# Kernel optimization log

Hardware: AMD Instinct MI355X
Metric: run time of the kernel (lower is better)

Reference implementation:

```python
import jax, jax.numpy as jnp
import numpy as np

IN_DIM, HID, OUT_DIM = 128, 24, 4096
B, K = 16384, 256

def setup_inputs() -> dict:
    key = jax.random.key(0)
    ks = jax.random.split(key, 8)
    x = jax.random.normal(ks[0], (B, IN_DIM), dtype=jnp.float32)
    possible_moves = jax.random.randint(ks[1], (B, K), 0, OUT_DIM)
    s1 = 1.0 / np.sqrt(IN_DIM)
    s2 = 1.0 / np.sqrt(HID)
    W1 = jax.random.uniform(ks[2], (IN_DIM, HID), jnp.float32, -s1, s1)
    b1 = jax.random.uniform(ks[3], (HID,), jnp.float32, -s1, s1)
    W2 = jax.random.uniform(ks[4], (HID, HID), jnp.float32, -s2, s2)
    b2 = jax.random.uniform(ks[5], (HID,), jnp.float32, -s2, s2)
    W3 = jax.random.uniform(ks[6], (HID, OUT_DIM), jnp.float32, -s2, s2)
    b3 = jax.random.uniform(ks[7], (OUT_DIM,), jnp.float32, -s2, s2)
    return {"x": x, "possible_moves": possible_moves,
            "W1": W1, "b1": b1, "W2": W2, "b2": b2, "W3": W3, "b3": b3}

def reference(x, possible_moves, W1, b1, W2, b2, W3, b3):
    # small MLP: 128 -> 24 -> 24 -> 4096
    h = jax.nn.relu(x @ W1 + b1)
    h = jax.nn.relu(h @ W2 + b2)
    logits = h @ W3 + b3                     # [B, OUT_DIM]
    # per-row legal-move mask via vectorized scatter (duplicates just re-set 1)
    Bn = logits.shape[0]
    rows = jnp.arange(Bn)[:, None]           # [B, 1] broadcasts over K
    mask = jnp.zeros_like(logits).at[rows, possible_moves].set(1.0)
    # faithful to original: multiply (not -inf) then softmax over full dim
    filtered = logits * mask
    return jax.nn.softmax(filtered, axis=1)
```

## Files before the change

kernel.cpp:

```cpp
#include <hip/hip_runtime.h>
#include <hip/hip_bf16.h>

#define IN_DIM 128
#define HID 24
#define OUT_DIM 4096
#define NB 16384
#define KMOV 256

#define TR_BLOCKS 384
#define MLP_BLOCKS (NB / 8)

__global__ __launch_bounds__(256) void kprep(const float* __restrict__ x,
                                             const float* __restrict__ W1,
                                             const float* __restrict__ b1,
                                             const float* __restrict__ W2,
                                             const float* __restrict__ b2,
                                             const float* __restrict__ W3,
                                             float* __restrict__ W3T,
                                             float* __restrict__ h2out) {
    __shared__ float W1s[IN_DIM * HID];
    __shared__ float W2s[HID * HID];
    __shared__ float b1s[HID], b2s[HID];
    __shared__ float xs[8][IN_DIM];

    int bid = blockIdx.x;
    int t = threadIdx.x;

    if (bid < TR_BLOCKS) {
        int i = bid * 256 + t;
        int c = i / HID;
        int k = i - c * HID;
        W3T[i] = W3[k * OUT_DIM + c];
        return;
    }

    for (int i = t; i < IN_DIM * HID; i += 256) W1s[i] = W1[i];
    for (int i = t; i < HID * HID; i += 256)    W2s[i] = W2[i];
    if (t < HID) { b1s[t] = b1[t]; b2s[t] = b2[t]; }
    int rbase = (bid - TR_BLOCKS) * 8;
    for (int i = t; i < 8 * IN_DIM; i += 256)
        xs[i >> 7][i & 127] = x[(size_t)rbase * IN_DIM + i];
    __syncthreads();

    int g = t >> 5;
    int j = t & 31;
    int r = rbase + g;

    float h1 = 0.f;
    if (j < HID) {
        h1 = b1s[j];
        #pragma unroll 8
        for (int i = 0; i < IN_DIM; i++) h1 += xs[g][i] * W1s[i * HID + j];
        h1 = fmaxf(h1, 0.f);
    }
    float h2 = (j < HID) ? b2s[j] : 0.f;
    #pragma unroll
    for (int k = 0; k < HID; k++) {
        float hk = __shfl(h1, k, 32);
        if (j < HID) h2 += hk * W2s[k * HID + j];
    }
    if (j < HID) {
        h2 = fmaxf(h2, 0.f);
        h2out[(size_t)r * HID + j] = h2;
    }
}

__global__ __launch_bounds__(256) void kmain2(const int* __restrict__ moves,
                                              const float* __restrict__ b3,
                                              const float* __restrict__ W3T,
                                              const float* __restrict__ h2all,
                                              float* __restrict__ out) {
    __shared__ __align__(16) float probs[OUT_DIM];
    __shared__ float h2s[HID];
    __shared__ float red[8];
    unsigned char* claimed = (unsigned char*)probs;

    int r = blockIdx.x;
    int t = threadIdx.x;

    int c = moves[(size_t)r * KMOV + t];
    if (t < HID) h2s[t] = h2all[(size_t)r * HID + t];
    __syncthreads();

    const float4* w = (const float4*)(W3T + c * HID);
    float4 a0 = w[0], a1 = w[1], a2 = w[2], a3 = w[3], a4 = w[4], a5 = w[5];
    float acc = b3[c];
    acc += a0.x*h2s[0] + a0.y*h2s[1] + a0.z*h2s[2]  + a0.w*h2s[3];
    acc += a1.x*h2s[4] + a1.y*h2s[5] + a1.z*h2s[6]  + a1.w*h2s[7];
    acc += a2.x*h2s[8] + a2.y*h2s[9] + a2.z*h2s[10] + a2.w*h2s[11];
    acc += a3.x*h2s[12]+ a3.y*h2s[13]+ a3.z*h2s[14] + a3.w*h2s[15];
    acc += a4.x*h2s[16]+ a4.y*h2s[17]+ a4.z*h2s[18] + a4.w*h2s[19];
    acc += a5.x*h2s[20]+ a5.y*h2s[21]+ a5.z*h2s[22] + a5.w*h2s[23];

    claimed[c] = (unsigned char)t;

    float m = acc;
    #pragma unroll
    for (int off = 32; off > 0; off >>= 1) m = fmaxf(m, __shfl_xor(m, off, 64));
    int wid = t >> 6;
    if ((t & 63) == 0) red[wid] = m;
    __syncthreads();
    float mm = fmaxf(fmaxf(fmaxf(red[0], red[1]), fmaxf(red[2], red[3])), 0.f);

    float e      = __expf(acc - mm);
    float base_e = __expf(-mm);

    float contrib = (claimed[c] == (unsigned char)t) ? (e - base_e) : 0.f;
    float s = contrib;
    #pragma unroll
    for (int off = 32; off > 0; off >>= 1) s += __shfl_xor(s, off, 64);
    if ((t & 63) == 0) red[4 + wid] = s;
    __syncthreads();
    float denom = (float)OUT_DIM * base_e + (red[4] + red[5] + red[6] + red[7]);
    float inv = 1.0f / denom;
    float oc  = base_e * inv;
    float pm  = e * inv;

    float4* p4 = (float4*)probs;
    float4 ocv = make_float4(oc, oc, oc, oc);
    #pragma unroll
    for (int i = 0; i < 4; i++) p4[t + i * 256] = ocv;
    __syncthreads();
    probs[c] = pm;
    __syncthreads();

    float4* out4 = (float4*)(out + (size_t)r * OUT_DIM);
    #pragma unroll
    for (int i = 0; i < 4; i++) out4[t + i * 256] = p4[t + i * 256];
}

extern "C" void kernel_launch(void* const* d_in, const int* in_sizes, int n_in,
                              void* d_out, int out_size, void* d_ws, size_t ws_size,
                              hipStream_t stream) {
    const float* x     = (const float*)d_in[0];
    const int*   moves = (const int*)  d_in[1];
    const float* W1    = (const float*)d_in[2];
    const float* b1    = (const float*)d_in[3];
    const float* W2    = (const float*)d_in[4];
    const float* b2    = (const float*)d_in[5];
    const float* W3    = (const float*)d_in[6];
    const float* b3    = (const float*)d_in[7];
    float* out = (float*)d_out;

    char* ws = (char*)d_ws;
    float* W3T = (float*)ws;
    float* h2  = (float*)(ws + OUT_DIM * HID * 4);

    kprep<<<TR_BLOCKS + MLP_BLOCKS, 256, 0, stream>>>(x, W1, b1, W2, b2, W3, W3T, h2);
    kmain2<<<NB, 256, 0, stream>>>(moves, b3, W3T, h2, out);
}
```

Measured before the change: 329.9 us.

## Dedupe moves via zeroed LDS scatter and store outputs nontemporally

Replaces the byte-claim dedup trick with zero-initialising the shared probability row, scattering exp(acc-max)-base per move, then having each thread read its float4 slice back to form the sum and the final output. This removes one barrier and the separate fill-then-scatter pass before the copy-out. Output writes now use nontemporal vector stores to avoid cache pollution for the large streaming output. It also moves the b3 load before the first barrier to overlap latency.

```diff
diff --git a/kernel.cpp b/kernel.cpp
--- a/kernel.cpp
+++ b/kernel.cpp
@@ -9,6 +9,8 @@
 
 #define TR_BLOCKS 384
 #define MLP_BLOCKS (NB / 8)
+
+typedef float f32x4 __attribute__((ext_vector_type(4)));
 
 __global__ __launch_bounds__(256) void kprep(const float* __restrict__ x,
                                              const float* __restrict__ W1,
@@ -73,26 +75,30 @@
     __shared__ __align__(16) float probs[OUT_DIM];
     __shared__ float h2s[HID];
     __shared__ float red[8];
-    unsigned char* claimed = (unsigned char*)probs;
 
     int r = blockIdx.x;
     int t = threadIdx.x;
 
     int c = moves[(size_t)r * KMOV + t];
     if (t < HID) h2s[t] = h2all[(size_t)r * HID + t];
-    __syncthreads();
 
     const float4* w = (const float4*)(W3T + c * HID);
     float4 a0 = w[0], a1 = w[1], a2 = w[2], a3 = w[3], a4 = w[4], a5 = w[5];
-    float acc = b3[c];
+    float bc = b3[c];
+    __syncthreads();
+
+    float4* p4 = (float4*)probs;
+    float4 z = make_float4(0.f, 0.f, 0.f, 0.f);
+    #pragma unroll
+    for (int i = 0; i < 4; i++) p4[t + i * 256] = z;
+
+    float acc = bc;
     acc += a0.x*h2s[0] + a0.y*h2s[1] + a0.z*h2s[2]  + a0.w*h2s[3];
     acc += a1.x*h2s[4] + a1.y*h2s[5] + a1.z*h2s[6]  + a1.w*h2s[7];
     acc += a2.x*h2s[8] + a2.y*h2s[9] + a2.z*h2s[10] + a2.w*h2s[11];
     acc += a3.x*h2s[12]+ a3.y*h2s[13]+ a3.z*h2s[14] + a3.w*h2s[15];
     acc += a4.x*h2s[16]+ a4.y*h2s[17]+ a4.z*h2s[18] + a4.w*h2s[19];
     acc += a5.x*h2s[20]+ a5.y*h2s[21]+ a5.z*h2s[22] + a5.w*h2s[23];
-
-    claimed[c] = (unsigned char)t;
 
     float m = acc;
     #pragma unroll
@@ -102,31 +108,33 @@
     __syncthreads();
     float mm = fmaxf(fmaxf(fmaxf(red[0], red[1]), fmaxf(red[2], red[3])), 0.f);
 
-    float e      = __expf(acc - mm);
     float base_e = __expf(-mm);
+    float em     = __expf(acc - mm) - base_e;
 
-    float contrib = (claimed[c] == (unsigned char)t) ? (e - base_e) : 0.f;
-    float s = contrib;
+    probs[c] = em;
+    __syncthreads();
+
+    float4 v0 = p4[t], v1 = p4[t + 256], v2 = p4[t + 512], v3 = p4[t + 768];
+    float s = (v0.x + v0.y + v0.z + v0.w) + (v1.x + v1.y + v1.z + v1.w)
+            + (v2.x + v2.y + v2.z + v2.w) + (v3.x + v3.y + v3.z + v3.w);
     #pragma unroll
     for (int off = 32; off > 0; off >>= 1) s += __shfl_xor(s, off, 64);
     if ((t & 63) == 0) red[4 + wid] = s;
     __syncthreads();
     float denom = (float)OUT_DIM * base_e + (red[4] + red[5] + red[6] + red[7]);
     float inv = 1.0f / denom;
-    float oc  = base_e * inv;
-    float pm  = e * inv;
 
-    float4* p4 = (float4*)probs;
-    float4 ocv = make_float4(oc, oc, oc, oc);
-    #pragma unroll
-    for (int i = 0; i < 4; i++) p4[t + i * 256] = ocv;
-    __syncthreads();
-    probs[c] = pm;
-    __syncthreads();
-
-    float4* out4 = (float4*)(out + (size_t)r * OUT_DIM);
-    #pragma unroll
-    for (int i = 0; i < 4; i++) out4[t + i * 256] = p4[t + i * 256];
+    f32x4* out4 = (f32x4*)(out + (size_t)r * OUT_DIM);
+    f32x4 r0, r1, r2, r3;
+    r0.x=(v0.x+base_e)*inv; r0.y=(v0.y+base_e)*inv; r0.z=(v0.z+base_e)*inv; r0.w=(v0.w+base_e)*inv;
+    r1.x=(v1.x+base_e)*inv; r1.y=(v1.y+base_e)*inv; r1.z=(v1.z+base_e)*inv; r1.w=(v1.w+base_e)*inv;
+    r2.x=(v2.x+base_e)*inv; r2.y=(v2.y+base_e)*inv; r2.z=(v2.z+base_e)*inv; r2.w=(v2.w+base_e)*inv;
+    r3.x=(v3.x+base_e)*inv; r3.y=(v3.y+base_e)*inv; r3.z=(v3.w+base_e)*inv; r3.w=(v3.w+base_e)*inv;
+    r3.z=(v3.z+base_e)*inv;
+    __builtin_nontemporal_store(r0, &out4[t]);
+    __builtin_nontemporal_store(r1, &out4[t + 256]);
+    __builtin_nontemporal_store(r2, &out4[t + 512]);
+    __builtin_nontemporal_store(r3, &out4[t + 768]);
 }
 
 extern "C" void kernel_launch(void* const* d_in, const int* in_sizes, int n_in,
```

Measured after the change: 351.2 us. +6.4%, slower.
